# Performance work log

Measured on AMD Instinct MI355X. Metric: run time of the kernel, lower is better.

The kernel has to match this reference:

```python
import jax, jax.numpy as jnp
import numpy as np

HIDDEN = 1000
DICT = 4811
T = 44
B = 256


def _lstm_cell(x, h, c, W_ih, W_hh, b_ih, b_hh):
    # gates: [B, 4*H], PyTorch order i, f, g, o
    gates = x @ W_ih.T + b_ih + h @ W_hh.T + b_hh
    i, f, g, o = jnp.split(gates, 4, axis=-1)
    i = jax.nn.sigmoid(i)
    f = jax.nn.sigmoid(f)
    g = jnp.tanh(g)
    o = jax.nn.sigmoid(o)
    c_new = f * c + i * g
    h_new = o * jnp.tanh(c_new)
    return h_new, c_new


def setup_inputs() -> dict:
    key = jax.random.key(0)
    ks = jax.random.split(key, 20)
    s = 0.02
    H = HIDDEN
    return {
        "x": jax.random.normal(ks[0], (B, T, H), jnp.float32),
        "h1": jax.random.normal(ks[1], (B, H), jnp.float32),
        "h2": jax.random.normal(ks[2], (B, H), jnp.float32),
        "c1": jax.random.normal(ks[3], (B, H), jnp.float32),
        "c2": jax.random.normal(ks[4], (B, H), jnp.float32),
        "layer_W": jax.random.normal(ks[5], (H, H), jnp.float32) * s,
        "layer_b": jnp.zeros((H,), jnp.float32),
        "W_ih1": jax.random.normal(ks[6], (4 * H, 2 * H), jnp.float32) * s,
        "W_hh1": jax.random.normal(ks[7], (4 * H, H), jnp.float32) * s,
        "b_ih1": jnp.zeros((4 * H,), jnp.float32),
        "b_hh1": jnp.zeros((4 * H,), jnp.float32),
        "W_ih2": jax.random.normal(ks[8], (4 * H, DICT + 2 * H), jnp.float32) * s,
        "W_hh2": jax.random.normal(ks[9], (4 * H, H), jnp.float32) * s,
        "b_ih2": jnp.zeros((4 * H,), jnp.float32),
        "b_hh2": jnp.zeros((4 * H,), jnp.float32),
        "out_W": jax.random.normal(ks[10], (DICT, H), jnp.float32) * s,
        "out_b": jnp.zeros((DICT,), jnp.float32),
    }


def reference(x, h1, h2, c1, c2, layer_W, layer_b,
              W_ih1, W_hh1, b_ih1, b_hh1,
              W_ih2, W_hh2, b_ih2, b_hh2,
              out_W, out_b):
    # input projection: [B, T, H]
    xp = x @ layer_W.T + layer_b
    prev0 = jnp.zeros((x.shape[0], DICT), x.dtype)

    def step(carry, xt):
        h1, c1, h2, c2, prev = carry
        l1_in = jnp.concatenate([xt, h1], axis=1)            # [B, 2H]
        h1n, c1n = _lstm_cell(l1_in, h1, c1, W_ih1, W_hh1, b_ih1, b_hh1)
        l2_in = jnp.concatenate([prev, h2, h1n], axis=1)     # [B, DICT+2H]
        h2n, c2n = _lstm_cell(l2_in, h2, c2, W_ih2, W_hh2, b_ih2, b_hh2)
        logits = h2n @ out_W.T + out_b                       # [B, DICT]
        # NOTE: original torch code softmaxes over dim=0 (batch axis)
        y = jax.nn.softmax(logits, axis=0)
        return (h1n, c1n, h2n, c2n, y), y

    xs = jnp.transpose(xp, (1, 0, 2))                        # [T, B, H]
    _, ys = jax.lax.scan(step, (h1, c1, h2, c2, prev0), xs)
    return jnp.transpose(ys, (1, 0, 2))                      # [B, T, DICT]
```

## Files before the change

kernel.cpp:

```cpp
#include <hip/hip_runtime.h>
#include <hip/hip_bf16.h>

#define HID   1000
#define DICT  4811
#define TT    44
#define BB    256
#define G4    4000
#define G4P   4096
#define K1P   2048
#define K2P   6912
#define HP    1024
#define Z2_H2 4864
#define Z2_H1 5888
#define PD    3
#define GPART ((long long)BB * G4P)

typedef __attribute__((ext_vector_type(8))) short short8;
typedef __attribute__((ext_vector_type(4))) float f32x4;

__device__ __forceinline__ short f2b(float f) {
    unsigned u = __float_as_uint(f);
    unsigned r = (u + 0x7FFFu + ((u >> 16) & 1u)) >> 16;
    return (short)r;
}

__device__ __forceinline__ void gload16(const void* g, const short* l) {
    __builtin_amdgcn_global_load_lds(
        (const __attribute__((address_space(1))) unsigned int*)g,
        (__attribute__((address_space(3))) unsigned int*)l, 16, 0, 0);
}

__global__ void prep_w1i(const float* __restrict__ wih1, const float* __restrict__ whh1,
                         short* __restrict__ w) {
    for (size_t i = (size_t)blockIdx.x * blockDim.x + threadIdx.x; i < (size_t)G4P * K1P;
         i += (size_t)gridDim.x * blockDim.x) {
        int n = (int)(i >> 11), j = (int)(i & 2047);
        int h = n >> 2, g = n & 3;
        float v = 0.f;
        if (h < HID) {
            int r = g * HID + h;
            if (j < HID) v = wih1[(size_t)r * 2000 + j];
            else if (j >= 1024 && j < 1024 + HID) {
                int jj = j - 1024;
                v = wih1[(size_t)r * 2000 + HID + jj] + whh1[(size_t)r * HID + jj];
            }
        }
        w[i] = f2b(v);
    }
}

__global__ void prep_w2p(const float* __restrict__ wih2, const float* __restrict__ whh2,
                         short* __restrict__ w) {
    int n = blockIdx.y;
    int j = blockIdx.x * 256 + threadIdx.x;
    float v = 0.f;
    if (n < G4) {
        if (j < DICT) v = wih2[(size_t)n * 6811 + j];
        else if (j >= Z2_H2 && j < Z2_H2 + HID) {
            int jj = j - Z2_H2;
            v = wih2[(size_t)n * 6811 + DICT + jj] + whh2[(size_t)n * HID + jj];
        } else if (j >= Z2_H1 && j < Z2_H1 + HID) {
            int jj = j - Z2_H1;
            v = wih2[(size_t)n * 6811 + DICT + HID + jj];
        }
    }
    w[(size_t)n * K2P + j] = f2b(v);
}

__global__ void prep_outwp(const float* __restrict__ outw, short* __restrict__ w) {
    int n = blockIdx.y;
    int j = blockIdx.x * 256 + threadIdx.x;
    float v = (n < DICT && j < HID) ? outw[(size_t)n * HID + j] : 0.f;
    w[(size_t)n * HP + j] = f2b(v);
}

__global__ void prep_cvt(const float* __restrict__ src, short* __restrict__ dst, size_t n) {
    for (size_t i = (size_t)blockIdx.x * blockDim.x + threadIdx.x; i < n;
         i += (size_t)gridDim.x * blockDim.x)
        dst[i] = f2b(src[i]);
}

__global__ void prep_addv(const float* __restrict__ a, const float* __restrict__ b,
                          float* __restrict__ dst, int n) {
    int i = blockIdx.x * blockDim.x + threadIdx.x;
    if (i < n) dst[i] = a[i] + b[i];
}

__global__ void prep_biasi(const float* __restrict__ bi, const float* __restrict__ bh,
                           float* __restrict__ dst) {
    int n = blockIdx.x * 256 + threadIdx.x;
    if (n >= 4096) return;
    int h = n >> 2, g = n & 3;
    dst[n] = (h < HID) ? bi[g * HID + h] + bh[g * HID + h] : 0.f;
}

__global__ void init_vec(const float* __restrict__ src, short* __restrict__ dst, int ld) {
    int i = blockIdx.x * blockDim.x + threadIdx.x;
    if (i >= BB * HID) return;
    int b = i / HID, h = i % HID;
    dst[(size_t)b * ld + h] = f2b(src[i]);
}

template <int EPI, int AF32>
__global__ __launch_bounds__(256) void gemm_nt(
    const void* __restrict__ Ap, int lda,
    const short* __restrict__ Bp, int ldb,
    const float* __restrict__ bias,
    void* __restrict__ Cp, long long partStride, int ldc,
    int M, int N, int Kvalid)
{
    __shared__ short As[64][40];
    __shared__ short Bs[64][40];
    const int tid  = threadIdx.x;
    const int lane = tid & 63;
    const int wave = tid >> 6;
    const int wm = wave >> 1, wn = wave & 1;
    const int tm = blockIdx.y * 64, tn = blockIdx.x * 64;
    const int srow = tid >> 2;
    const int scol = (tid & 3) * 8;

    const int nk = (Kvalid + 31) >> 5;
    const int s0 = (int)(((long long)nk * blockIdx.z) / gridDim.z);
    const int s1 = (int)(((long long)nk * (blockIdx.z + 1)) / gridDim.z);

    const int arow = tm + srow;
    const int brow = tn + srow;
    const bool bvalid = brow < N;

    auto loadA = [&](int ks) -> short8 {
        int k = (ks << 5) + scol;
        short8 r = {0, 0, 0, 0, 0, 0, 0, 0};
        if (k + 8 <= Kvalid) {
            if (AF32) {
                const f32x4* p = (const f32x4*)((const float*)Ap + (size_t)arow * lda + k);
                f32x4 u0 = p[0], u1 = p[1];
                r[0] = f2b(u0[0]); r[1] = f2b(u0[1]); r[2] = f2b(u0[2]); r[3] = f2b(u0[3]);
                r[4] = f2b(u1[0]); r[5] = f2b(u1[1]); r[6] = f2b(u1[2]); r[7] = f2b(u1[3]);
            } else {
                r = *(const short8*)((const short*)Ap + (size_t)arow * lda + k);
            }
        }
        return r;
    };
    auto loadB = [&](int ks) -> short8 {
        int k = (ks << 5) + scol;
        short8 r = {0, 0, 0, 0, 0, 0, 0, 0};
        if (bvalid && (k + 8 <= Kvalid))
            r = *(const short8*)(Bp + (size_t)brow * ldb + k);
        return r;
    };

    f32x4 acc[2][2];
    for (int a = 0; a < 2; ++a)
        for (int b = 0; b < 2; ++b)
            acc[a][b] = (f32x4){0.f, 0.f, 0.f, 0.f};

    short8 ra = loadA(s0), rb = loadB(s0);
    *(short8*)&As[srow][scol] = ra;
    *(short8*)&Bs[srow][scol] = rb;
    __syncthreads();

    const int kg = (lane >> 4) * 8;
    const int fr = lane & 15;

    for (int s = s0; s < s1; ++s) {
        short8 a0 = *(short8*)&As[wm * 32 + fr][kg];
        short8 a1 = *(short8*)&As[wm * 32 + 16 + fr][kg];
        short8 b0 = *(short8*)&Bs[wn * 32 + fr][kg];
        short8 b1 = *(short8*)&Bs[wn * 32 + 16 + fr][kg];
        short8 na, nb;
        if (s + 1 < s1) { na = loadA(s + 1); nb = loadB(s + 1); }
        acc[0][0] = __builtin_amdgcn_mfma_f32_16x16x32_bf16(a0, b0, acc[0][0], 0, 0, 0);
        acc[0][1] = __builtin_amdgcn_mfma_f32_16x16x32_bf16(a0, b1, acc[0][1], 0, 0, 0);
        acc[1][0] = __builtin_amdgcn_mfma_f32_16x16x32_bf16(a1, b0, acc[1][0], 0, 0, 0);
        acc[1][1] = __builtin_amdgcn_mfma_f32_16x16x32_bf16(a1, b1, acc[1][1], 0, 0, 0);
        __syncthreads();
        if (s + 1 < s1) {
            *(short8*)&As[srow][scol] = na;
            *(short8*)&Bs[srow][scol] = nb;
        }
        __syncthreads();
    }

    float* Cf = (float*)Cp + (size_t)partStride * blockIdx.z;
    for (int mi = 0; mi < 2; ++mi)
        for (int ni = 0; ni < 2; ++ni) {
            int col = tn + wn * 32 + ni * 16 + (lane & 15);
            if (col >= N) continue;
            float bv = bias ? bias[col] : 0.f;
            int row0 = tm + wm * 32 + mi * 16 + ((lane >> 4) << 2);
            f32x4 v = acc[mi][ni];
            for (int j = 0; j < 4; ++j) {
                int row = row0 + j;
                float val = v[j] + bv;
                if (EPI == 0) {
                    Cf[(size_t)row * ldc + col] = val;
                } else {
                    int b = row / TT, t = row % TT;
                    ((short*)Cp)[((size_t)t * BB + b) * ldc + col] = f2b(val);
                }
            }
        }
}

__device__ __forceinline__ void gates1F_dev(short* smem, int bx, int by,
    const short* __restrict__ xp_t,
    const short* __restrict__ h1m,
    const short* __restrict__ w1i,
    const f32x4* __restrict__ bias4,
    float* __restrict__ c1,
    short* __restrict__ zh1,
    short* __restrict__ h1nxt)
{
    const int tid  = threadIdx.x;
    const int lane = tid & 63;
    const int w    = tid >> 6;
    const int wm = w >> 1, wn = w & 1;
    const int tm = by * 64;
    const int tn = bx * 64;
    const int nk = K1P / 32;

    const int rA = tid >> 2, sl = tid & 3;
    const int swz = (sl ^ ((rA >> 1) & 3)) << 3;
    const size_t aoff = (size_t)(tm + rA) * HP + (size_t)swz;
    const size_t boff = (size_t)(tn + rA) * K1P + (size_t)swz;

    auto stage = [&](int buf, int s) {
        const int k0 = s << 5;
        const short* As = (k0 < 1024) ? xp_t : h1m;
        const short* l = smem + buf * 4096;
        gload16(As + k0 + aoff, l + tid * 8);
        gload16(w1i + k0 + boff, l + 2048 + tid * 8);
    };

    const int fr = lane & 15;
    const int kg = lane >> 4;
    int aRd[2], bRd[2];
    #pragma unroll
    for (int mi = 0; mi < 2; ++mi) {
        int row = wm * 32 + mi * 16 + fr;
        aRd[mi] = row * 32 + ((kg ^ ((row >> 1) & 3)) << 3);
    }
    #pragma unroll
    for (int ni = 0; ni < 2; ++ni) {
        int row = wn * 32 + ni * 16 + fr;
        bRd[ni] = 2048 + row * 32 + ((kg ^ ((row >> 1) & 3)) << 3);
    }

    f32x4 acc[2][2];
    #pragma unroll
    for (int a = 0; a < 2; ++a)
        #pragma unroll
        for (int b = 0; b < 2; ++b)
            acc[a][b] = (f32x4){0.f, 0.f, 0.f, 0.f};

    #pragma unroll
    for (int i = 0; i < PD; ++i) stage(i, i);

    int buf = 0;
    for (int s = 0; s < nk; ++s) {
        const int ahead = nk - 1 - s;
        if (ahead >= 2)      asm volatile("s_waitcnt vmcnt(4)" ::: "memory");
        else if (ahead == 1) asm volatile("s_waitcnt vmcnt(2)" ::: "memory");
        else                 asm volatile("s_waitcnt vmcnt(0)" ::: "memory");
        __builtin_amdgcn_s_barrier();

        const short* bp = smem + buf * 4096;
        short8 af[2], bf[2];
        #pragma unroll
        for (int i = 0; i < 2; ++i) af[i] = *(const short8*)(bp + aRd[i]);
        #pragma unroll
        for (int i = 0; i < 2; ++i) bf[i] = *(const short8*)(bp + bRd[i]);
        asm volatile("s_waitcnt lgkmcnt(0)" ::: "memory");
        __builtin_amdgcn_sched_barrier(0);
        __builtin_amdgcn_s_barrier();
        if (s + PD < nk) stage(buf, s + PD);

        #pragma unroll
        for (int mi = 0; mi < 2; ++mi)
            #pragma unroll
            for (int ni = 0; ni < 2; ++ni)
                acc[mi][ni] = __builtin_amdgcn_mfma_f32_16x16x32_bf16(af[mi], bf[ni], acc[mi][ni], 0, 0, 0);

        buf = (buf + 1 == PD) ? 0 : buf + 1;
    }

    float* gl = (float*)smem;
    #pragma unroll
    for (int mi = 0; mi < 2; ++mi)
        #pragma unroll
        for (int ni = 0; ni < 2; ++ni) {
            int row = wm * 32 + mi * 16 + kg * 4;
            int col = wn * 32 + ni * 16 + fr;
            #pragma unroll
            for (int j = 0; j < 4; ++j)
                gl[(row + j) * 68 + col] = acc[mi][ni][j];
        }
    __syncthreads();

    const int b_loc = tid & 63;
    const int b_g = tm + b_loc;
    #pragma unroll
    for (int q = 0; q < 4; ++q) {
        int h_loc = (tid >> 6) * 4 + q;
        int h_g = bx * 16 + h_loc;
        if (h_g >= HID) continue;
        f32x4 g4 = *(const f32x4*)(gl + b_loc * 68 + h_loc * 4);
        g4 += bias4[h_g];
        float ii = 1.f / (1.f + expf(-g4[0]));
        float ff = 1.f / (1.f + expf(-g4[1]));
        float tg = tanhf(g4[2]);
        float oo = 1.f / (1.f + expf(-g4[3]));
        float cn = ff * c1[(size_t)b_g * HID + h_g] + ii * tg;
        c1[(size_t)b_g * HID + h_g] = cn;
        short hb = f2b(oo * tanhf(cn));
        zh1[(size_t)b_g * K2P + h_g] = hb;
        h1nxt[(size_t)b_g * HP + h_g] = hb;
    }
}

__global__ __launch_bounds__(256) void gates1F(
    const short* __restrict__ xp_t, const short* __restrict__ h1m,
    const short* __restrict__ w1i, const f32x4* __restrict__ bias4,
    float* __restrict__ c1, short* __restrict__ zh1, short* __restrict__ h1nxt)
{
    __shared__ __align__(16) short smem[PD * 4096];
    gates1F_dev(smem, blockIdx.x, blockIdx.y, xp_t, h1m, w1i, bias4, c1, zh1, h1nxt);
}

__device__ __forceinline__ void lstm2_dev(int blk,
    const float* __restrict__ g, const float* __restrict__ bias, float* __restrict__ c,
    short* __restrict__ d1, int ld1, short* __restrict__ d2, int ld2)
{
    int i = blk * 256 + threadIdx.x;
    if (i >= BB * HID) return;
    int b = i / HID, h = i % HID;
    size_t base = (size_t)b * G4P + h;
    float gi = bias[h], gf = bias[HID + h], gg = bias[2 * HID + h], go = bias[3 * HID + h];
    #pragma unroll
    for (int p = 0; p < 8; ++p) {
        const float* gp = g + (size_t)GPART * p + base;
        gi += gp[0];
        gf += gp[HID];
        gg += gp[2 * HID];
        go += gp[3 * HID];
    }
    float ii = 1.f / (1.f + expf(-gi));
    float ff = 1.f / (1.f + expf(-gf));
    float tg = tanhf(gg);
    float oo = 1.f / (1.f + expf(-go));
    float cn = ff * c[i] + ii * tg;
    c[i] = cn;
    float hn = oo * tanhf(cn);
    short hb = f2b(hn);
    d1[(size_t)b * ld1 + h] = hb;
    d2[(size_t)b * ld2 + h] = hb;
}

__global__ __launch_bounds__(256) void fusedC(
    const short* __restrict__ xp_t1, const short* __restrict__ h1m,
    const short* __restrict__ w1i, const f32x4* __restrict__ bi1,
    float* __restrict__ c1, short* __restrict__ zh1, short* __restrict__ h1nxt,
    const float* __restrict__ gbuf, const float* __restrict__ bias2,
    float* __restrict__ c2, short* __restrict__ zh2, short* __restrict__ h2pad)
{
    __shared__ __align__(16) short smem[PD * 4096];
    const int x = blockIdx.x;
    if (x < 256)
        gates1F_dev(smem, x & 63, x >> 6, xp_t1, h1m, w1i, bi1, c1, zh1, h1nxt);
    else
        lstm2_dev(x - 256, gbuf, bias2, c2, zh2, K2P, h2pad, HP);
}

__global__ __launch_bounds__(512, 4) void gemm_s128(
    const short* __restrict__ A0, const short* __restrict__ A1, int splitA, int lda,
    const short* __restrict__ Bw, int ldb,
    float* __restrict__ C, long long partStride, int ldc, int nk)
{
    __shared__ __align__(16) short smem[PD][8192];
    const int tid  = threadIdx.x;
    const int lane = tid & 63;
    const int w    = tid >> 6;
    const int wm = w >> 2, wn = w & 3;
    const int tm = blockIdx.y * 128;
    const int tn = blockIdx.x * 128;
    const int s0 = (int)(((long long)nk * blockIdx.z) / gridDim.z);
    const int s1 = (int)(((long long)nk * (blockIdx.z + 1)) / gridDim.z);

    const int rA = tid >> 2, slA = tid & 3;
    const int swz = (slA ^ ((rA >> 1) & 3)) << 3;
    const size_t aoff = (size_t)(tm + rA) * lda + (size_t)swz;
    const size_t boff = (size_t)(tn + rA) * ldb + (size_t)swz;

    auto stage = [&](int buf, int s) {
        const int k0 = s << 5;
        const short* As = (k0 < splitA) ? A0 : A1;
        const short* l = &smem[buf][0];
        gload16(As + k0 + aoff, l + tid * 8);
        gload16(Bw + k0 + boff, l + 4096 + tid * 8);
    };

    const int fr = lane & 15;
    const int kg = lane >> 4;
    int aRd[4], bRd[2];
    #pragma unroll
    for (int mi = 0; mi < 4; ++mi) {
        int row = wm * 64 + mi * 16 + fr;
        aRd[mi] = row * 32 + ((kg ^ ((row >> 1) & 3)) << 3);
    }
    #pragma unroll
    for (int ni = 0; ni < 2; ++ni) {
        int row = wn * 32 + ni * 16 + fr;
        bRd[ni] = 4096 + row * 32 + ((kg ^ ((row >> 1) & 3)) << 3);
    }

    f32x4 acc[4][2];
    #pragma unroll
    for (int a = 0; a < 4; ++a)
        #pragma unroll
        for (int b = 0; b < 2; ++b)
            acc[a][b] = (f32x4){0.f, 0.f, 0.f, 0.f};

    #pragma unroll
    for (int i = 0; i < PD; ++i)
        if (s0 + i < s1) stage(i, s0 + i);

    int buf = 0;
    for (int s = s0; s < s1; ++s) {
        const int ahead = s1 - 1 - s;
        if (ahead >= 2)      asm volatile("s_waitcnt vmcnt(4)" ::: "memory");
        else if (ahead == 1) asm volatile("s_waitcnt vmcnt(2)" ::: "memory");
        else                 asm volatile("s_waitcnt vmcnt(0)" ::: "memory");
        __builtin_amdgcn_s_barrier();

        const short* bp = &smem[buf][0];
        short8 af[4], bf[2];
        #pragma unroll
        for (int i = 0; i < 4; ++i) af[i] = *(const short8*)(bp + aRd[i]);
        #pragma unroll
        for (int i = 0; i < 2; ++i) bf[i] = *(const short8*)(bp + bRd[i]);
        asm volatile("s_waitcnt lgkmcnt(0)" ::: "memory");
        __builtin_amdgcn_sched_barrier(0);
        __builtin_amdgcn_s_barrier();
        if (s + PD < s1) stage(buf, s + PD);

        #pragma unroll
        for (int mi = 0; mi < 4; ++mi)
            #pragma unroll
            for (int ni = 0; ni < 2; ++ni)
                acc[mi][ni] = __builtin_amdgcn_mfma_f32_16x16x32_bf16(af[mi], bf[ni], acc[mi][ni], 0, 0, 0);

        buf = (buf + 1 == PD) ? 0 : buf + 1;
    }

    float* Cp = C + (size_t)partStride * blockIdx.z;
    const int colb = tn + wn * 32 + fr;
    const int rowb = tm + wm * 64 + (kg << 2);
    #pragma unroll
    for (int mi = 0; mi < 4; ++mi)
        #pragma unroll
        for (int ni = 0; ni < 2; ++ni) {
            int col = colb + ni * 16;
            int row0 = rowb + mi * 16;
            #pragma unroll
            for (int j = 0; j < 4; ++j)
                Cp[(size_t)(row0 + j) * ldc + col] = acc[mi][ni][j];
        }
}

__global__ __launch_bounds__(512) void logits_sm(
    const short* __restrict__ A , const short* __restrict__ Bw ,
    const float* __restrict__ outb, float* __restrict__ out,
    short* __restrict__ z2, int t)
{
    __shared__ __align__(16) short smem[PD][10240];
    __shared__ float red[256];
    const int tid  = threadIdx.x;
    const int lane = tid & 63;
    const int w    = tid >> 6;
    const int wm = w >> 1, wn = w & 1;
    const int tn = blockIdx.x * 64;
    const int nk = HP / 32;

    const int cA0 = w * 64 + lane;
    const int cA1 = cA0 + 512;
    const int rA0 = cA0 >> 2, rA1 = cA1 >> 2;
    const size_t aoff0 = (size_t)rA0 * HP + (size_t)((((cA0 & 3) ^ ((rA0 >> 1) & 3))) << 3);
    const size_t aoff1 = (size_t)rA1 * HP + (size_t)((((cA1 & 3) ^ ((rA1 >> 1) & 3))) << 3);
    const int cB = w * 32 + (lane & 31);
    const int rB = cB >> 2;
    const size_t boff = (size_t)(tn + rB) * HP + (size_t)((((cB & 3) ^ ((rB >> 1) & 3))) << 3);

    auto stage = [&](int buf, int s) {
        const int k0 = s << 5;
        const short* l = &smem[buf][0];
        gload16(A + k0 + aoff0, l + w * 512);
        gload16(A + k0 + aoff1, l + 4096 + w * 512);
        if (lane < 32) gload16(Bw + k0 + boff, l + 8192 + w * 256);
    };

    const int fr = lane & 15;
    const int kg = lane >> 4;
    int aRd[4], bRd[2];
    #pragma unroll
    for (int mi = 0; mi < 4; ++mi) {
        int row = wm * 64 + mi * 16 + fr;
        aRd[mi] = row * 32 + ((kg ^ ((row >> 1) & 3)) << 3);
    }
    #pragma unroll
    for (int ni = 0; ni < 2; ++ni) {
        int row = wn * 32 + ni * 16 + fr;
        bRd[ni] = 8192 + row * 32 + ((kg ^ ((row >> 1) & 3)) << 3);
    }

    f32x4 acc[4][2];
    #pragma unroll
    for (int a = 0; a < 4; ++a)
        #pragma unroll
        for (int b = 0; b < 2; ++b)
            acc[a][b] = (f32x4){0.f, 0.f, 0.f, 0.f};

    #pragma unroll
    for (int i = 0; i < PD; ++i) stage(i, i);

    int buf = 0;
    for (int s = 0; s < nk; ++s) {
        const int ahead = nk - 1 - s;
        if (ahead >= 2)      asm volatile("s_waitcnt vmcnt(6)" ::: "memory");
        else if (ahead == 1) asm volatile("s_waitcnt vmcnt(3)" ::: "memory");
        else                 asm volatile("s_waitcnt vmcnt(0)" ::: "memory");
        __builtin_amdgcn_s_barrier();

        const short* bp = &smem[buf][0];
        short8 af[4], bf[2];
        #pragma unroll
        for (int i = 0; i < 4; ++i) af[i] = *(const short8*)(bp + aRd[i]);
        #pragma unroll
        for (int i = 0; i < 2; ++i) bf[i] = *(const short8*)(bp + bRd[i]);
        asm volatile("s_waitcnt lgkmcnt(0)" ::: "memory");
        __builtin_amdgcn_sched_barrier(0);
        __builtin_amdgcn_s_barrier();
        if (s + PD < nk) stage(buf, s + PD);

        #pragma unroll
        for (int mi = 0; mi < 4; ++mi)
            #pragma unroll
            for (int ni = 0; ni < 2; ++ni)
                acc[mi][ni] = __builtin_amdgcn_mfma_f32_16x16x32_bf16(af[mi], bf[ni], acc[mi][ni], 0, 0, 0);

        buf = (buf + 1 == PD) ? 0 : buf + 1;
    }

    int   colv[2];
    float bv[2];
    #pragma unroll
    for (int ni = 0; ni < 2; ++ni) {
        colv[ni] = tn + wn * 32 + ni * 16 + fr;
        bv[ni] = (colv[ni] < DICT) ? outb[colv[ni]] : 0.f;
    }
    float v[4][2][4];
    float mx[2] = {-3e38f, -3e38f};
    #pragma unroll
    for (int mi = 0; mi < 4; ++mi)
        #pragma unroll
        for (int ni = 0; ni < 2; ++ni)
            #pragma unroll
            for (int j = 0; j < 4; ++j) {
                float x = acc[mi][ni][j] + bv[ni];
                v[mi][ni][j] = x;
                mx[ni] = fmaxf(mx[ni], x);
            }
    #pragma unroll
    for (int ni = 0; ni < 2; ++ni) {
        mx[ni] = fmaxf(mx[ni], __shfl_xor(mx[ni], 16));
        mx[ni] = fmaxf(mx[ni], __shfl_xor(mx[ni], 32));
    }
    if (lane < 16) {
        red[wm * 64 + wn * 32 + fr]      = mx[0];
        red[wm * 64 + wn * 32 + 16 + fr] = mx[1];
    }
    __syncthreads();
    float m[2];
    #pragma unroll
    for (int ni = 0; ni < 2; ++ni) {
        int cc = wn * 32 + ni * 16 + fr;
        m[ni] = fmaxf(fmaxf(red[cc], red[64 + cc]), fmaxf(red[128 + cc], red[192 + cc]));
    }
    __syncthreads();
    float s2[2] = {0.f, 0.f};
    #pragma unroll
    for (int mi = 0; mi < 4; ++mi)
        #pragma unroll
        for (int ni = 0; ni < 2; ++ni)
            #pragma unroll
            for (int j = 0; j < 4; ++j) {
                float e = expf(v[mi][ni][j] - m[ni]);
                v[mi][ni][j] = e;
                s2[ni] += e;
            }
    #pragma unroll
    for (int ni = 0; ni < 2; ++ni) {
        s2[ni] += __shfl_xor(s2[ni], 16);
        s2[ni] += __shfl_xor(s2[ni], 32);
    }
    if (lane < 16) {
        red[wm * 64 + wn * 32 + fr]      = s2[0];
        red[wm * 64 + wn * 32 + 16 + fr] = s2[1];
    }
    __syncthreads();
    float inv[2];
    #pragma unroll
    for (int ni = 0; ni < 2; ++ni) {
        int cc = wn * 32 + ni * 16 + fr;
        inv[ni] = 1.f / (red[cc] + red[64 + cc] + red[128 + cc] + red[192 + cc]);
    }
    const int rowb = wm * 64 + (kg << 2);
    #pragma unroll
    for (int mi = 0; mi < 4; ++mi)
        #pragma unroll
        for (int j = 0; j < 4; ++j) {
            int b = rowb + mi * 16 + j;
            #pragma unroll
            for (int ni = 0; ni < 2; ++ni) {
                if (colv[ni] < DICT) {
                    float y = v[mi][ni][j] * inv[ni];
                    out[(size_t)b * ((size_t)TT * DICT) + (size_t)t * DICT + colv[ni]] = y;
                    z2[(size_t)b * K2P + colv[ni]] = f2b(y);
                }
            }
        }
}

extern "C" void kernel_launch(void* const* d_in, const int* in_sizes, int n_in,
                              void* d_out, int out_size, void* d_ws, size_t ws_size,
                              hipStream_t stream)
{
    const float* x    = (const float*)d_in[0];
    const float* h1   = (const float*)d_in[1];
    const float* h2   = (const float*)d_in[2];
    const float* c1in = (const float*)d_in[3];
    const float* c2in = (const float*)d_in[4];
    const float* layW = (const float*)d_in[5];
    const float* layb = (const float*)d_in[6];
    const float* Wih1 = (const float*)d_in[7];
    const float* Whh1 = (const float*)d_in[8];
    const float* bih1 = (const float*)d_in[9];
    const float* bhh1 = (const float*)d_in[10];
    const float* Wih2 = (const float*)d_in[11];
    const float* Whh2 = (const float*)d_in[12];
    const float* bih2 = (const float*)d_in[13];
    const float* bhh2 = (const float*)d_in[14];
    const float* outW = (const float*)d_in[15];
    const float* outb = (const float*)d_in[16];
    float* out = (float*)d_out;
    (void)in_sizes; (void)n_in; (void)out_size; (void)ws_size;

    char* ws = (char*)d_ws;
    size_t off = 0;
    auto alloc = [&](size_t bytes) -> void* {
        size_t p = off;
        off = (off + bytes + 255) & ~(size_t)255;
        return (void*)(ws + p);
    };

    short* w1i   = (short*)alloc((size_t)G4P * K1P * 2);
    short* w2cat = (short*)alloc((size_t)G4P * K2P * 2);
    short* outwb = (short*)alloc((size_t)4864 * HP * 2);
    short* laywb = (short*)alloc((size_t)HID * HID * 2);
    short* xp    = (short*)alloc((size_t)TT * BB * HP * 2);
    short* h1A   = (short*)alloc((size_t)BB * HP * 2);
    short* h1B   = (short*)alloc((size_t)BB * HP * 2);
    short* h2pad = (short*)alloc((size_t)BB * HP * 2);
    short* z2    = (short*)alloc((size_t)BB * K2P * 2);
    float* gbuf  = (float*)alloc((size_t)8 * BB * G4P * 4);
    float* c1    = (float*)alloc((size_t)BB * HID * 4);
    float* c2    = (float*)alloc((size_t)BB * HID * 4);
    float* bi1   = (float*)alloc((size_t)G4P * 4);
    float* bias2 = (float*)alloc((size_t)G4 * 4);

    hipMemsetAsync(xp, 0, (size_t)TT * BB * HP * 2, stream);
    hipMemsetAsync(z2, 0, (size_t)BB * K2P * 2, stream);
    hipMemsetAsync(h1A, 0, (size_t)BB * HP * 2, stream);
    hipMemsetAsync(h1B, 0, (size_t)BB * HP * 2, stream);
    hipMemsetAsync(h2pad, 0, (size_t)BB * HP * 2, stream);

    prep_w1i<<<4096, 256, 0, stream>>>(Wih1, Whh1, w1i);
    prep_w2p<<<dim3(27, G4P), 256, 0, stream>>>(Wih2, Whh2, w2cat);
    prep_outwp<<<dim3(4, 4864), 256, 0, stream>>>(outW, outwb);
    prep_cvt<<<1024, 256, 0, stream>>>(layW, laywb, (size_t)HID * HID);
    prep_biasi<<<16, 256, 0, stream>>>(bih1, bhh1, bi1);
    prep_addv<<<16, 256, 0, stream>>>(bih2, bhh2, bias2, G4);
    init_vec<<<1000, 256, 0, stream>>>(h1, h1A, HP);
    init_vec<<<1000, 256, 0, stream>>>(h2, h2pad, HP);
    init_vec<<<1000, 256, 0, stream>>>(h2, z2 + Z2_H2, K2P);
    hipMemcpyAsync(c1, c1in, (size_t)BB * HID * 4, hipMemcpyDeviceToDevice, stream);
    hipMemcpyAsync(c2, c2in, (size_t)BB * HID * 4, hipMemcpyDeviceToDevice, stream);

    gemm_nt<1, 1><<<dim3(16, (BB * TT) / 64, 1), 256, 0, stream>>>(
        x, HID, laywb, HID, layb, xp, 0, HP, BB * TT, HID, HID);

    gates1F<<<dim3(64, 4), 256, 0, stream>>>(
        xp, h1A - HP, w1i, (const f32x4*)bi1, c1, z2 + Z2_H1, h1B);

    for (int t = 0; t < TT; ++t) {
        short* hcur = (t & 1) ? h1A : h1B;
        short* hnxt = (t & 1) ? h1B : h1A;
        int tn1 = (t + 1 < TT) ? (t + 1) : (TT - 1);

        gemm_s128<<<dim3(32, 2, 8), 512, 0, stream>>>(
            z2, z2, 0, K2P, w2cat, K2P, gbuf, GPART, G4P, K2P / 32);

        fusedC<<<1256, 256, 0, stream>>>(
            xp + (size_t)tn1 * BB * HP, hcur - HP, w1i, (const f32x4*)bi1,
            c1, z2 + Z2_H1, hnxt,
            gbuf, bias2, c2, z2 + Z2_H2, h2pad);

        logits_sm<<<76, 512, 0, stream>>>(h2pad, outwb, outb, out, z2, t);
    }
}
```

Measured before the change: 3.385 ms.

## Replace split-K gate2 GEMM with full-M 256x64 tiles and 4-way split

Replaces the layer-2 gate GEMM, which used 128x128 tiles with 8-way split-K over 512 blocks, with a kernel whose tiles cover all 256 batch rows and 64 gate columns, split 4 ways over K. Each weight tile is now streamed once per step instead of once per M-block, and the number of fp32 partial-sum buffers written and then summed in lstm2 drops from 8 to 4. The trade-off is fewer blocks (256 rather than 512), so each CU has less parallelism and fewer waves to hide latency. Each block also needs a larger shared-memory tile.

Result: slower. 3.456 ms (+2.1%).

```diff
diff --git a/kernel.cpp b/kernel.cpp
--- a/kernel.cpp
+++ b/kernel.cpp
@@ -338,7 +338,7 @@
     size_t base = (size_t)b * G4P + h;
     float gi = bias[h], gf = bias[HID + h], gg = bias[2 * HID + h], go = bias[3 * HID + h];
     #pragma unroll
-    for (int p = 0; p < 8; ++p) {
+    for (int p = 0; p < 4; ++p) {
         const float* gp = g + (size_t)GPART * p + base;
         gi += gp[0];
         gf += gp[HID];
@@ -372,32 +372,34 @@
         lstm2_dev(x - 256, gbuf, bias2, c2, zh2, K2P, h2pad, HP);
 }
 
-__global__ __launch_bounds__(512, 4) void gemm_s128(
-    const short* __restrict__ A0, const short* __restrict__ A1, int splitA, int lda,
-    const short* __restrict__ Bw, int ldb,
-    float* __restrict__ C, long long partStride, int ldc, int nk)
+__global__ __launch_bounds__(512) void gates2_fullM(
+    const short* __restrict__ A , const short* __restrict__ Bw ,
+    float* __restrict__ C, int nkTot)
 {
-    __shared__ __align__(16) short smem[PD][8192];
+    __shared__ __align__(16) short smem[PD][10240];
     const int tid  = threadIdx.x;
     const int lane = tid & 63;
     const int w    = tid >> 6;
-    const int wm = w >> 2, wn = w & 3;
-    const int tm = blockIdx.y * 128;
-    const int tn = blockIdx.x * 128;
-    const int s0 = (int)(((long long)nk * blockIdx.z) / gridDim.z);
-    const int s1 = (int)(((long long)nk * (blockIdx.z + 1)) / gridDim.z);
-
-    const int rA = tid >> 2, slA = tid & 3;
-    const int swz = (slA ^ ((rA >> 1) & 3)) << 3;
-    const size_t aoff = (size_t)(tm + rA) * lda + (size_t)swz;
-    const size_t boff = (size_t)(tn + rA) * ldb + (size_t)swz;
+    const int wm = w >> 1, wn = w & 1;
+    const int tn = blockIdx.x * 64;
+    const int s0 = (int)(((long long)nkTot * blockIdx.z) / gridDim.z);
+    const int s1 = (int)(((long long)nkTot * (blockIdx.z + 1)) / gridDim.z);
+
+    const int cA0 = w * 64 + lane;
+    const int cA1 = cA0 + 512;
+    const int rA0 = cA0 >> 2, rA1 = cA1 >> 2;
+    const size_t aoff0 = (size_t)rA0 * K2P + (size_t)((((cA0 & 3) ^ ((rA0 >> 1) & 3))) << 3);
+    const size_t aoff1 = (size_t)rA1 * K2P + (size_t)((((cA1 & 3) ^ ((rA1 >> 1) & 3))) << 3);
+    const int cB = w * 32 + (lane & 31);
+    const int rB = cB >> 2;
+    const size_t boff = (size_t)(tn + rB) * K2P + (size_t)((((cB & 3) ^ ((rB >> 1) & 3))) << 3);
 
     auto stage = [&](int buf, int s) {
         const int k0 = s << 5;
-        const short* As = (k0 < splitA) ? A0 : A1;
         const short* l = &smem[buf][0];
-        gload16(As + k0 + aoff, l + tid * 8);
-        gload16(Bw + k0 + boff, l + 4096 + tid * 8);
+        gload16(A + k0 + aoff0, l + w * 512);
+        gload16(A + k0 + aoff1, l + 4096 + w * 512);
+        if (lane < 32) gload16(Bw + k0 + boff, l + 8192 + w * 256);
     };
 
     const int fr = lane & 15;
@@ -411,7 +413,7 @@
     #pragma unroll
     for (int ni = 0; ni < 2; ++ni) {
         int row = wn * 32 + ni * 16 + fr;
-        bRd[ni] = 4096 + row * 32 + ((kg ^ ((row >> 1) & 3)) << 3);
+        bRd[ni] = 8192 + row * 32 + ((kg ^ ((row >> 1) & 3)) << 3);
     }
 
     f32x4 acc[4][2];
@@ -428,8 +430,8 @@
     int buf = 0;
     for (int s = s0; s < s1; ++s) {
         const int ahead = s1 - 1 - s;
-        if (ahead >= 2)      asm volatile("s_waitcnt vmcnt(4)" ::: "memory");
-        else if (ahead == 1) asm volatile("s_waitcnt vmcnt(2)" ::: "memory");
+        if (ahead >= 2)      asm volatile("s_waitcnt vmcnt(6)" ::: "memory");
+        else if (ahead == 1) asm volatile("s_waitcnt vmcnt(3)" ::: "memory");
         else                 asm volatile("s_waitcnt vmcnt(0)" ::: "memory");
         __builtin_amdgcn_s_barrier();
 
@@ -453,9 +455,9 @@
         buf = (buf + 1 == PD) ? 0 : buf + 1;
     }
 
-    float* Cp = C + (size_t)partStride * blockIdx.z;
+    float* Cp = C + (size_t)GPART * blockIdx.z;
     const int colb = tn + wn * 32 + fr;
-    const int rowb = tm + wm * 64 + (kg << 2);
+    const int rowb = wm * 64 + (kg << 2);
     #pragma unroll
     for (int mi = 0; mi < 4; ++mi)
         #pragma unroll
@@ -464,7 +466,7 @@
             int row0 = rowb + mi * 16;
             #pragma unroll
             for (int j = 0; j < 4; ++j)
-                Cp[(size_t)(row0 + j) * ldc + col] = acc[mi][ni][j];
+                Cp[(size_t)(row0 + j) * G4P + col] = acc[mi][ni][j];
         }
 }
 
@@ -672,7 +674,7 @@
     short* h1B   = (short*)alloc((size_t)BB * HP * 2);
     short* h2pad = (short*)alloc((size_t)BB * HP * 2);
     short* z2    = (short*)alloc((size_t)BB * K2P * 2);
-    float* gbuf  = (float*)alloc((size_t)8 * BB * G4P * 4);
+    float* gbuf  = (float*)alloc((size_t)4 * BB * G4P * 4);
     float* c1    = (float*)alloc((size_t)BB * HID * 4);
     float* c2    = (float*)alloc((size_t)BB * HID * 4);
     float* bi1   = (float*)alloc((size_t)G4P * 4);
@@ -707,8 +709,8 @@
         short* hnxt = (t & 1) ? h1B : h1A;
         int tn1 = (t + 1 < TT) ? (t + 1) : (TT - 1);
 
-        gemm_s128<<<dim3(32, 2, 8), 512, 0, stream>>>(
-            z2, z2, 0, K2P, w2cat, K2P, gbuf, GPART, G4P, K2P / 32);
+        gates2_fullM<<<dim3(64, 1, 4), 512, 0, stream>>>(
+            z2, w2cat, gbuf, K2P / 32);
 
         fusedC<<<1256, 256, 0, stream>>>(
             xp + (size_t)tn1 * BB * HP, hcur - HP, w1i, (const f32x4*)bi1,
```
